# Kernel optimization log

Measured on AMD Instinct MI355X. Metric: run time of the kernel, lower is better.

Reference implementation:

```python
import jax, jax.numpy as jnp
import numpy as np

NMS_THR = 0.3


def pairwise_iou(b):
    # b: [N,4] in x1,y1,x2,y2
    area = (b[:, 2] - b[:, 0]) * (b[:, 3] - b[:, 1])  # [N]
    x1 = jnp.maximum(b[:, None, 0], b[None, :, 0])
    y1 = jnp.maximum(b[:, None, 1], b[None, :, 1])
    x2 = jnp.minimum(b[:, None, 2], b[None, :, 2])
    y2 = jnp.minimum(b[:, None, 3], b[None, :, 3])
    inter = jnp.clip(x2 - x1, 0.0) * jnp.clip(y2 - y1, 0.0)
    return inter / (area[:, None] + area[None, :] - inter + 1e-9)


def nms_keep(boxes, scores, valid, thr):
    # greedy NMS, fixed-shape: returns bool keep mask in original order
    N = boxes.shape[0]
    order = jnp.argsort(-jnp.where(valid, scores, -jnp.inf))
    b = boxes[order]
    v = valid[order]
    iou = pairwise_iou(b)  # [N,N]

    def step(keep, i):
        suppressed = jnp.any(keep & (iou[i] > thr))
        keep = keep.at[i].set(v[i] & jnp.logical_not(suppressed))
        return keep, None

    keep_sorted, _ = jax.lax.scan(step, jnp.zeros((N,), dtype=bool), jnp.arange(N))
    return jnp.zeros((N,), dtype=bool).at[order].set(keep_sorted)


def setup_inputs() -> dict:
    key = jax.random.key(0)
    k1, k2, k3, k4 = jax.random.split(key, 4)
    N, C, S = 6000, 81, 800
    # well-formed proposals: x1,y1 in [0, 600), w,h in [8, 200)
    xy = jax.random.uniform(k1, (N, 2), dtype=jnp.float32) * 600.0
    wh = 8.0 + jax.random.uniform(k2, (N, 2), dtype=jnp.float32) * 192.0
    proposals = jnp.concatenate([xy, xy + wh], axis=1)  # [N,4]
    reg = jax.random.normal(k3, (N, C * 4), dtype=jnp.float32)
    clss = jax.random.normal(k4, (N, C), dtype=jnp.float32) * 2.0
    stds = jnp.array([0.1, 0.1, 0.2, 0.2], dtype=jnp.float32)
    return {"proposals": proposals, "reg": reg, "clss": clss, "stds": stds, "img_size": S}


def reference(proposals, reg, clss, stds, img_size):
    N, C = clss.shape
    # anchors_bbox2offset: x1y1x2y2 -> center x,y + w,h
    w = proposals[:, 2] - proposals[:, 0]
    h = proposals[:, 3] - proposals[:, 1]
    cx = proposals[:, 0] + 0.5 * w
    cy = proposals[:, 1] + 0.5 * h
    # class selection
    probs = jax.nn.softmax(clss, axis=1)
    cls_idx = jnp.argmax(probs, axis=1)  # [N]
    score = jnp.take_along_axis(probs, cls_idx[:, None], axis=1)[:, 0]
    valid = cls_idx != 0  # non-background
    reg4 = reg.reshape(N, C, 4)
    t = jnp.take_along_axis(reg4, cls_idx[:, None, None], axis=1)[:, 0, :] * stds  # [N,4]
    # decode
    px = cx + w * t[:, 0]
    py = cy + h * t[:, 1]
    pw = w * jnp.exp(t[:, 2])
    ph = h * jnp.exp(t[:, 3])
    # offset2bbox + clip
    hi = jnp.float32(img_size - 1)
    x1 = jnp.clip(px - 0.5 * pw, 0.0, hi)
    y1 = jnp.clip(py - 0.5 * ph, 0.0, hi)
    x2 = jnp.clip(px + 0.5 * pw, 0.0, hi)
    y2 = jnp.clip(py + 0.5 * ph, 0.0, hi)
    boxes = jnp.stack((x1, y1, x2, y2), axis=1)  # [N,4]
    keep = nms_keep(jax.lax.stop_gradient(boxes), jax.lax.stop_gradient(score), valid, NMS_THR)
    m = keep.astype(boxes.dtype)
    return boxes * m[:, None], score * m, cls_idx * keep.astype(cls_idx.dtype)
```

## Files before the change

### kernel.cpp

```cpp
#include <hip/hip_runtime.h>
#include <math.h>

#define NMS_THR 0.3f
#define NACC 8

__device__ __forceinline__ float fmul(float a, float b){ return __fmul_rn(a,b); }
__device__ __forceinline__ float fadd(float a, float b){ return __fadd_rn(a,b); }
__device__ __forceinline__ float fsub(float a, float b){ return __fsub_rn(a,b); }

#define BAR_LDS() asm volatile("s_waitcnt lgkmcnt(0)\n\ts_barrier" ::: "memory")

__device__ __forceinline__ unsigned long long rdlane64(unsigned long long v, int a) {
    unsigned long long l = (unsigned int)__builtin_amdgcn_readlane((int)(unsigned int)v, a);
    unsigned long long h = (unsigned int)__builtin_amdgcn_readlane((int)(unsigned int)(v >> 32), a);
    return (h << 32) | l;
}
__device__ __forceinline__ unsigned long long rfl64(unsigned long long x){
    unsigned int lo = (unsigned int)__builtin_amdgcn_readfirstlane((int)(unsigned int)x);
    unsigned int hi = (unsigned int)__builtin_amdgcn_readfirstlane((int)(unsigned int)(x >> 32));
    return ((unsigned long long)hi << 32) | lo;
}
__device__ __forceinline__ unsigned long long waveOr64(unsigned long long v){
    for (int o = 32; o > 0; o >>= 1) v |= __shfl_xor(v, o);
    return v;
}

__global__ __launch_bounds__(256) void k_decode(
    const float* __restrict__ prop, const float* __restrict__ reg,
    const float* __restrict__ clss, const float* __restrict__ stds,
    const int* __restrict__ imgsz,
    float* __restrict__ boxes, float* __restrict__ key,
    float* __restrict__ score, int* __restrict__ cls,
    int N, int C)
{
    int wid  = threadIdx.x >> 6;
    int lane = threadIdx.x & 63;
    int n = blockIdx.x * 4 + wid;
    if (n >= N) return;
    const float* row = clss + (long)n * C;
    float ninf = -__builtin_inff();
    float x0 = (lane < C)      ? row[lane]      : ninf;
    float x1 = (lane + 64 < C) ? row[lane + 64] : ninf;
    float m = fmaxf(x0, x1);
    for (int o = 32; o > 0; o >>= 1) m = fmaxf(m, __shfl_xor(m, o));
    float e0 = (lane < C)      ? expf(x0 - m) : 0.0f;
    float e1 = (lane + 64 < C) ? expf(x1 - m) : 0.0f;
    float s = e0 + e1;
    for (int o = 32; o > 0; o >>= 1) s += __shfl_xor(s, o);
    float bv; int bi;
    if (e0 >= e1) { bv = e0; bi = lane; } else { bv = e1; bi = lane + 64; }
    for (int o = 32; o > 0; o >>= 1) {
        float ov = __shfl_xor(bv, o);
        int   oi = __shfl_xor(bi, o);
        if (ov > bv || (ov == bv && oi < bi)) { bv = ov; bi = oi; }
    }
    if (lane == 0) {
        float sc = 1.0f / s;
        int   c  = bi;
        int   valid = (c != 0);
        float p0 = prop[n*4+0], p1 = prop[n*4+1], p2 = prop[n*4+2], p3 = prop[n*4+3];
        float w  = fsub(p2, p0), h = fsub(p3, p1);
        float cx = fadd(p0, fmul(0.5f, w));
        float cy = fadd(p1, fmul(0.5f, h));
        const float* rr = reg + (long)n * C * 4 + (long)c * 4;
        float t0 = fmul(rr[0], stds[0]);
        float t1 = fmul(rr[1], stds[1]);
        float t2 = fmul(rr[2], stds[2]);
        float t3 = fmul(rr[3], stds[3]);
        float px = fadd(cx, fmul(w, t0));
        float py = fadd(cy, fmul(h, t1));
        float pw = fmul(w, expf(t2));
        float ph = fmul(h, expf(t3));
        float hi = (float)(imgsz[0] - 1);
        float bx1 = fminf(fmaxf(fsub(px, fmul(0.5f, pw)), 0.0f), hi);
        float by1 = fminf(fmaxf(fsub(py, fmul(0.5f, ph)), 0.0f), hi);
        float bx2 = fminf(fmaxf(fadd(px, fmul(0.5f, pw)), 0.0f), hi);
        float by2 = fminf(fmaxf(fadd(py, fmul(0.5f, ph)), 0.0f), hi);
        boxes[n*4+0]=bx1; boxes[n*4+1]=by1; boxes[n*4+2]=bx2; boxes[n*4+3]=by2;
        score[n] = sc;
        cls[n]   = c;
        key[n]   = valid ? sc : ninf;
    }
}

__global__ __launch_bounds__(256) void k_rank(
    const float* __restrict__ key, const float* __restrict__ boxes,
    float* __restrict__ boxesSorted, float* __restrict__ areaSorted,
    float* __restrict__ keySorted, int* __restrict__ rank,
    int* __restrict__ nValidPtr, int N)
{
    extern __shared__ float lkey[];
    __shared__ int part[256];
    int tid = threadIdx.x;
    for (int j = tid; j < N; j += 256) lkey[j] = key[j];
    __syncthreads();

    int i = blockIdx.x * 64 + (tid & 63);
    int s = tid >> 6;
    int Q = (N + 3) >> 2;
    int r_part = 0;
    if (i < N) {
        float ki = lkey[i];
        int j0 = s * Q, j1 = min(N, j0 + Q);
        for (int j = j0; j < j1; ++j) {
            float kj = lkey[j];
            r_part += (kj > ki) || (kj == ki && j < i);
        }
    }
    part[tid] = r_part;
    __syncthreads();

    if (tid < 64 && i < N) {
        int r = part[tid] + part[tid+64] + part[tid+128] + part[tid+192];
        float ki = lkey[i];
        rank[i] = r;
        float b0 = boxes[i*4+0], b1 = boxes[i*4+1], b2 = boxes[i*4+2], b3 = boxes[i*4+3];
        boxesSorted[r*4+0]=b0; boxesSorted[r*4+1]=b1; boxesSorted[r*4+2]=b2; boxesSorted[r*4+3]=b3;
        areaSorted[r] = fmul(fsub(b2,b0), fsub(b3,b1));
        keySorted[r]  = ki;
    }

    if (blockIdx.x == 0) {
        __syncthreads();
        float ninf = -__builtin_inff();
        int inv = 0;
        for (int j = tid; j < N; j += 256) inv += (lkey[j] == ninf);
        part[tid] = inv;
        __syncthreads();
        if (tid == 0) {
            int t = 0;
            for (int q = 0; q < 256; ++q) t += part[q];
            nValidPtr[0] = N - t;
        }
    }
}

__global__ __launch_bounds__(256) void k_mask(
    const float* __restrict__ bs, const float* __restrict__ areas,
    const float* __restrict__ keySorted, unsigned long long* __restrict__ mask,
    unsigned long long* __restrict__ dq,
    int N, int W, int Wpad)
{
    int wid  = threadIdx.x >> 6;
    int lane = threadIdx.x & 63;
    int i = blockIdx.x * 4 + wid;
    if (i >= N) return;
    if (keySorted[i] == -__builtin_inff()) return;
    float ax1 = bs[i*4+0], ay1 = bs[i*4+1], ax2 = bs[i*4+2], ay2 = bs[i*4+3];
    float aa  = areas[i];
    int w0 = i >> 6;
    if (lane == 0) {
        dq[i*4+0] = 0ULL; dq[i*4+1] = 0ULL; dq[i*4+2] = 0ULL; dq[i*4+3] = 0ULL;
    }
    for (int w = w0; w < W; ++w) {
        int j = w*64 + lane;
        int bit = 0;
        if (j < N && j > i) {
            float bx1 = bs[j*4+0], by1 = bs[j*4+1], bx2 = bs[j*4+2], by2 = bs[j*4+3];
            float ba  = areas[j];
            float ix1 = fmaxf(ax1,bx1), iy1 = fmaxf(ay1,by1);
            float ix2 = fminf(ax2,bx2), iy2 = fminf(ay2,by2);
            float iw = fmaxf(fsub(ix2,ix1), 0.0f);
            float ih = fmaxf(fsub(iy2,iy1), 0.0f);
            float inter = fmul(iw, ih);
            float denom = fadd(fsub(fadd(aa, ba), inter), 1e-9f);
            float iou = inter / denom;
            bit = (iou > NMS_THR) ? 1 : 0;
        }
        unsigned long long bm = __ballot(bit);
        if (lane == 0) {
            mask[(long)i*Wpad + w] = bm;
            int d = w - w0;
            if (d < 4) dq[i*4+d] = bm;
        }
    }
}

__global__ __launch_bounds__((NACC+1)*64, 1) void k_scan(
    const unsigned long long* __restrict__ mask,
    const unsigned long long* __restrict__ dq,
    const int* __restrict__ nValidPtr,
    int* __restrict__ keepSorted,
    const float* __restrict__ boxes, const float* __restrict__ score,
    const int* __restrict__ cls, const int* __restrict__ rank,
    float* __restrict__ out,
    int N, int W, int Wpad)
{
    __shared__ unsigned long long ldsPartA[NACC+1];
    __shared__ unsigned long long ldsPartB[NACC+1];
    __shared__ unsigned long long ldsKeepLo, ldsKeepHi;
    int tid  = threadIdx.x;
    int wid  = tid >> 6;
    int lane = tid & 63;
    for (int i = tid; i < N; i += (NACC+1)*64) keepSorted[i] = 0;
    if (tid <= NACC) { ldsPartA[tid] = 0ULL; ldsPartB[tid] = 0ULL; }
    if (tid == 0) { ldsKeepLo = 0ULL; ldsKeepHi = 0ULL; }
    __syncthreads();

    int nValid  = __builtin_amdgcn_readfirstlane(nValidPtr[0]);
    int nChunks = (nValid + 127) >> 7;

    unsigned long long A0=0,A1=0,A2=0,A3=0,B0=0,B1=0,B2=0,B3=0;
    unsigned long long sacc_prevA = 0ULL, sacc_prevB = 0ULL;
    if (wid == 0 && nChunks > 0) {
        int rA = lane, rB = 64 + lane;
        if (rA < N) {
            ulonglong2 a01 = *(const ulonglong2*)(dq + (size_t)rA*4);
            ulonglong2 a23 = *(const ulonglong2*)(dq + (size_t)rA*4 + 2);
            A0=a01.x; A1=a01.y; A2=a23.x; A3=a23.y;
        }
        if (rB < N) {
            ulonglong2 b01 = *(const ulonglong2*)(dq + (size_t)rB*4);
            ulonglong2 b23 = *(const ulonglong2*)(dq + (size_t)rB*4 + 2);
            B0=b01.x; B1=b01.y; B2=b23.x; B3=b23.y;
        }
    }
    unsigned long long accx = 0ULL, accy = 0ULL;
    bool accWave = (wid >= 1);
    int  accIdx  = wid - 1;
    bool laneok  = (2*lane + 1 < Wpad);

    for (int c = 0; c < nChunks; ++c) {
        int base = c << 7;
        if (wid == 0) {
            unsigned long long nA0=0,nA1=0,nA2=0,nA3=0,nB0=0,nB1=0,nB2=0,nB3=0;
            if (c + 1 < nChunks) {
                int rA = base + 128 + lane, rB = base + 192 + lane;
                if (rA < N) {
                    ulonglong2 a01 = *(const ulonglong2*)(dq + (size_t)rA*4);
                    ulonglong2 a23 = *(const ulonglong2*)(dq + (size_t)rA*4 + 2);
                    nA0=a01.x; nA1=a01.y; nA2=a23.x; nA3=a23.y;
                }
                if (rB < N) {
                    ulonglong2 b01 = *(const ulonglong2*)(dq + (size_t)rB*4);
                    ulonglong2 b23 = *(const ulonglong2*)(dq + (size_t)rB*4 + 2);
                    nB0=b01.x; nB1=b01.y; nB2=b23.x; nB3=b23.y;
                }
            }

            unsigned long long pA = sacc_prevA, pB = sacc_prevB;
#pragma unroll
            for (int k = 1; k <= NACC; ++k) { pA |= ldsPartA[k]; pB |= ldsPartB[k]; }
            unsigned long long incLo = rfl64(pA), incHi = rfl64(pB);
            int nv  = nValid - base;
            unsigned long long validLo = (nv >= 64) ? ~0ULL : ((1ULL << nv) - 1ULL);
            int nv2 = nv - 64;
            unsigned long long validHi = (nv2 >= 64) ? ~0ULL
                                        : (nv2 <= 0 ? 0ULL : ((1ULL << nv2) - 1ULL));
            unsigned long long candLo = validLo & ~incLo;
            unsigned long long candHi = validHi & ~incHi;
            unsigned long long keepLo = 0ULL, keepHi = 0ULL;

            while (candLo) {
                int a = __builtin_ctzll(candLo);
                unsigned long long bit = 1ULL << a;
                keepLo |= bit;
                candLo &= ~bit & ~rdlane64(A0, a);
            }
            {
                unsigned long long sel = ((keepLo >> lane) & 1ULL) ? A1 : 0ULL;
                candHi &= ~waveOr64(sel);
            }
            while (candHi) {
                int a = __builtin_ctzll(candHi);
                unsigned long long bit = 1ULL << a;
                keepHi |= bit;
                candHi &= ~bit & ~rdlane64(B0, a);
            }
            {
                unsigned long long kL = (keepLo >> lane) & 1ULL;
                unsigned long long kH = (keepHi >> lane) & 1ULL;
                unsigned long long selA = (kL ? A2 : 0ULL) | (kH ? B1 : 0ULL);
                unsigned long long selB = (kL ? A3 : 0ULL) | (kH ? B2 : 0ULL);
                sacc_prevA = waveOr64(selA);
                sacc_prevB = waveOr64(selB);
            }
            if (lane == 0) { ldsKeepLo = keepLo; ldsKeepHi = keepHi; }
            if (base + lane < N)      keepSorted[base + lane]      = (int)((keepLo >> lane) & 1ULL);
            if (base + 64 + lane < N) keepSorted[base + 64 + lane] = (int)((keepHi >> lane) & 1ULL);
            A0=nA0; A1=nA1; A2=nA2; A3=nA3; B0=nB0; B1=nB1; B2=nB2; B3=nB3;
        }
        BAR_LDS();
        unsigned long long kLo = ldsKeepLo;
        unsigned long long kHi = ldsKeepHi;
        if (accWave && laneok && lane == c + 1) {
            ldsPartA[wid] = accx;
            ldsPartB[wid] = accy;
        }
        BAR_LDS();
        if (accWave && laneok) {
            unsigned int myb = (accIdx < 4)
                ? (unsigned int)((kLo >> (16*accIdx)) & 0xFFFFULL)
                : (unsigned int)((kHi >> (16*(accIdx-4))) & 0xFFFFULL);
            if (myb) {
                const unsigned long long* mb =
                    mask + (size_t)(base + 16*accIdx) * Wpad + 2*lane;
                unsigned int b = myb;
                int a0 = __builtin_ctz(b); b &= b - 1;
                int a1 = -1, a2 = -1, a3 = -1;
                if (b) { a1 = __builtin_ctz(b); b &= b - 1; }
                if (b) { a2 = __builtin_ctz(b); b &= b - 1; }
                if (b) { a3 = __builtin_ctz(b); b &= b - 1; }
                ulonglong2 v0 = {0,0}, v1 = {0,0}, v2 = {0,0}, v3 = {0,0};
                v0 = *(const ulonglong2*)(mb + (size_t)a0 * Wpad);
                if (a1 >= 0) v1 = *(const ulonglong2*)(mb + (size_t)a1 * Wpad);
                if (a2 >= 0) v2 = *(const ulonglong2*)(mb + (size_t)a2 * Wpad);
                if (a3 >= 0) v3 = *(const ulonglong2*)(mb + (size_t)a3 * Wpad);
                accx |= (v0.x | v1.x) | (v2.x | v3.x);
                accy |= (v0.y | v1.y) | (v2.y | v3.y);
                while (b) {
                    int a = __builtin_ctz(b); b &= b - 1;
                    ulonglong2 v = *(const ulonglong2*)(mb + (size_t)a * Wpad);
                    accx |= v.x; accy |= v.y;
                }
            }
        }
    }

    __syncthreads();
    for (int n = tid; n < N; n += (NACC+1)*64) {
        int k = keepSorted[rank[n]];
        float m = (float)k;
        out[n*4+0] = boxes[n*4+0]*m;
        out[n*4+1] = boxes[n*4+1]*m;
        out[n*4+2] = boxes[n*4+2]*m;
        out[n*4+3] = boxes[n*4+3]*m;
        out[(long)N*4 + n] = score[n]*m;
        out[(long)N*5 + n] = (float)(cls[n] * k);
    }
}

extern "C" void kernel_launch(void* const* d_in, const int* in_sizes, int n_in,
                              void* d_out, int out_size, void* d_ws, size_t ws_size,
                              hipStream_t stream) {
    const float* prop = (const float*)d_in[0];
    const float* reg  = (const float*)d_in[1];
    const float* clss = (const float*)d_in[2];
    const float* stds = (const float*)d_in[3];
    const int*   img  = (const int*)d_in[4];

    int N = in_sizes[0] / 4;
    int C = in_sizes[2] / N;
    int W = (N + 63) / 64;
    int Wpad = (W + 1) & ~1;

    char* ws = (char*)d_ws;
    size_t off = 0;
    float* boxes       = (float*)(ws + off); off += (size_t)N*4*sizeof(float);
    float* key         = (float*)(ws + off); off += (size_t)N*sizeof(float);
    float* score       = (float*)(ws + off); off += (size_t)N*sizeof(float);
    int*   cls         = (int*)  (ws + off); off += (size_t)N*sizeof(int);
    int*   rank        = (int*)  (ws + off); off += (size_t)N*sizeof(int);
    float* boxesSorted = (float*)(ws + off); off += (size_t)N*4*sizeof(float);
    float* areaSorted  = (float*)(ws + off); off += (size_t)N*sizeof(float);
    float* keySorted   = (float*)(ws + off); off += (size_t)N*sizeof(float);
    int*   keepSorted  = (int*)  (ws + off); off += (size_t)N*sizeof(int);
    int*   nValid      = (int*)  (ws + off); off += sizeof(int);
    off = (off + 31) & ~(size_t)31;
    unsigned long long* dq    = (unsigned long long*)(ws + off);
    off += (size_t)N * 4 * sizeof(unsigned long long);
    unsigned long long* mask  = (unsigned long long*)(ws + off);
    off += (size_t)N * Wpad * sizeof(unsigned long long);
    (void)ws_size; (void)out_size; (void)n_in;

    int rowBlocks  = (N + 3) / 4;
    int rankBlocks = (N + 63) / 64;

    k_decode<<<rowBlocks, 256, 0, stream>>>(prop, reg, clss, stds, img,
                                            boxes, key, score, cls, N, C);
    k_rank<<<rankBlocks, 256, (size_t)N*sizeof(float), stream>>>(key, boxes,
                                            boxesSorted, areaSorted, keySorted, rank, nValid, N);
    k_mask<<<rowBlocks, 256, 0, stream>>>(boxesSorted, areaSorted, keySorted,
                                          mask, dq, N, W, Wpad);
    k_scan<<<1, (NACC+1)*64, 0, stream>>>(mask, dq, nValid, keepSorted,
                                          boxes, score, cls, rank, (float*)d_out,
                                          N, W, Wpad);
}
```

Before: 200.5 us.

## Batch four candidates per greedy step and split output write into separate kernel

The serial greedy loop inside the single-block scan now takes up to four candidate bits per iteration and reads their suppression rows with independent readlanes. This shortens the dependent latency chain for each kept box. The cross-half suppression is now built from readlanes of A1 in the same loop, replacing the wave-wide OR reduction. The final masked output write moves from the single-block scan kernel to a new grid-wide kernel, so it runs across all CUs, at the cost of one extra launch.

Result: faster. 187.2 us (-6.6%).

```diff
diff --git a/kernel.cpp b/kernel.cpp
--- a/kernel.cpp
+++ b/kernel.cpp
@@ -180,11 +180,7 @@
     const unsigned long long* __restrict__ mask,
     const unsigned long long* __restrict__ dq,
     const int* __restrict__ nValidPtr,
-    int* __restrict__ keepSorted,
-    const float* __restrict__ boxes, const float* __restrict__ score,
-    const int* __restrict__ cls, const int* __restrict__ rank,
-    float* __restrict__ out,
-    int N, int W, int Wpad)
+    int* __restrict__ keepSorted, int N, int W, int Wpad)
 {
     __shared__ unsigned long long ldsPartA[NACC+1];
     __shared__ unsigned long long ldsPartB[NACC+1];
@@ -251,21 +247,44 @@
             unsigned long long candHi = validHi & ~incHi;
             unsigned long long keepLo = 0ULL, keepHi = 0ULL;
 
+            unsigned long long mHiAcc = 0ULL;
             while (candLo) {
-                int a = __builtin_ctzll(candLo);
-                unsigned long long bit = 1ULL << a;
-                keepLo |= bit;
-                candLo &= ~bit & ~rdlane64(A0, a);
+                unsigned long long t = candLo;
+                int a0 = __builtin_ctzll(t); t &= t - 1;
+                int a1 = t ? __builtin_ctzll(t) : a0; t &= t - 1;
+                int a2 = t ? __builtin_ctzll(t) : a0; t &= t - 1;
+                int a3 = t ? __builtin_ctzll(t) : a0;
+                unsigned long long m0 = rdlane64(A0, a0), m1 = rdlane64(A0, a1);
+                unsigned long long m2 = rdlane64(A0, a2), m3 = rdlane64(A0, a3);
+                unsigned long long n0 = rdlane64(A1, a0), n1 = rdlane64(A1, a1);
+                unsigned long long n2 = rdlane64(A1, a2), n3 = rdlane64(A1, a3);
+                unsigned long long rem  = m0 | (1ULL << a0);
+                unsigned long long kept = 1ULL << a0;
+                unsigned long long hi   = n0;
+                unsigned long long b;
+                b = 1ULL << a1; if (!(rem & b)) { rem |= m1 | b; kept |= b; hi |= n1; }
+                b = 1ULL << a2; if (!(rem & b)) { rem |= m2 | b; kept |= b; hi |= n2; }
+                b = 1ULL << a3; if (!(rem & b)) { rem |= m3 | b; kept |= b; hi |= n3; }
+                keepLo |= kept; mHiAcc |= hi;
+                candLo &= ~rem;
             }
-            {
-                unsigned long long sel = ((keepLo >> lane) & 1ULL) ? A1 : 0ULL;
-                candHi &= ~waveOr64(sel);
-            }
+            candHi &= ~mHiAcc;
             while (candHi) {
-                int a = __builtin_ctzll(candHi);
-                unsigned long long bit = 1ULL << a;
-                keepHi |= bit;
-                candHi &= ~bit & ~rdlane64(B0, a);
+                unsigned long long t = candHi;
+                int a0 = __builtin_ctzll(t); t &= t - 1;
+                int a1 = t ? __builtin_ctzll(t) : a0; t &= t - 1;
+                int a2 = t ? __builtin_ctzll(t) : a0; t &= t - 1;
+                int a3 = t ? __builtin_ctzll(t) : a0;
+                unsigned long long m0 = rdlane64(B0, a0), m1 = rdlane64(B0, a1);
+                unsigned long long m2 = rdlane64(B0, a2), m3 = rdlane64(B0, a3);
+                unsigned long long rem  = m0 | (1ULL << a0);
+                unsigned long long kept = 1ULL << a0;
+                unsigned long long b;
+                b = 1ULL << a1; if (!(rem & b)) { rem |= m1 | b; kept |= b; }
+                b = 1ULL << a2; if (!(rem & b)) { rem |= m2 | b; kept |= b; }
+                b = 1ULL << a3; if (!(rem & b)) { rem |= m3 | b; kept |= b; }
+                keepHi |= kept;
+                candHi &= ~rem;
             }
             {
                 unsigned long long kL = (keepLo >> lane) & 1ULL;
@@ -316,18 +335,24 @@
             }
         }
     }
-
-    __syncthreads();
-    for (int n = tid; n < N; n += (NACC+1)*64) {
-        int k = keepSorted[rank[n]];
-        float m = (float)k;
-        out[n*4+0] = boxes[n*4+0]*m;
-        out[n*4+1] = boxes[n*4+1]*m;
-        out[n*4+2] = boxes[n*4+2]*m;
-        out[n*4+3] = boxes[n*4+3]*m;
-        out[(long)N*4 + n] = score[n]*m;
-        out[(long)N*5 + n] = (float)(cls[n] * k);
-    }
+}
+
+__global__ __launch_bounds__(256) void k_out(
+    const float* __restrict__ boxes, const float* __restrict__ score,
+    const int* __restrict__ cls, const int* __restrict__ rank,
+    const int* __restrict__ keepSorted,
+    float* __restrict__ out, int N)
+{
+    int n = blockIdx.x * blockDim.x + threadIdx.x;
+    if (n >= N) return;
+    int k = keepSorted[rank[n]];
+    float m = (float)k;
+    out[n*4+0] = boxes[n*4+0]*m;
+    out[n*4+1] = boxes[n*4+1]*m;
+    out[n*4+2] = boxes[n*4+2]*m;
+    out[n*4+3] = boxes[n*4+3]*m;
+    out[(long)N*4 + n] = score[n]*m;
+    out[(long)N*5 + n] = (float)(cls[n] * k);
 }
 
 extern "C" void kernel_launch(void* const* d_in, const int* in_sizes, int n_in,
@@ -364,6 +389,7 @@
     (void)ws_size; (void)out_size; (void)n_in;
 
     int rowBlocks  = (N + 3) / 4;
+    int thrBlocks  = (N + 255) / 256;
     int rankBlocks = (N + 63) / 64;
 
     k_decode<<<rowBlocks, 256, 0, stream>>>(prop, reg, clss, stds, img,
@@ -372,7 +398,7 @@
                                             boxesSorted, areaSorted, keySorted, rank, nValid, N);
     k_mask<<<rowBlocks, 256, 0, stream>>>(boxesSorted, areaSorted, keySorted,
                                           mask, dq, N, W, Wpad);
-    k_scan<<<1, (NACC+1)*64, 0, stream>>>(mask, dq, nValid, keepSorted,
-                                          boxes, score, cls, rank, (float*)d_out,
-                                          N, W, Wpad);
-}
+    k_scan<<<1, (NACC+1)*64, 0, stream>>>(mask, dq, nValid, keepSorted, N, W, Wpad);
+    k_out<<<thrBlocks, 256, 0, stream>>>(boxes, score, cls, rank, keepSorted,
+                                         (float*)d_out, N);
+}
```
